# Performance work log

Hardware: AMD Instinct MI355X
Metric: run time of the kernel (lower is better)

The kernel has to match this reference:

```python
import jax, jax.numpy as jnp
import numpy as np

B, N, C = 2, 1024, 768
H = 12            # num_heads
HP = 24           # H_prime
HD = C // H       # head_dim = 64
KS = 3            # local conv kernel size
SCALE = HD ** -0.5


def setup_inputs() -> dict:
    key = jax.random.key(0)
    ks = jax.random.split(key, 9)
    s = lambda fan_in: 1.0 / np.sqrt(fan_in)
    return {
        "x": jax.random.normal(ks[0], (B, N, C), jnp.float32),
        "W_qk": jax.random.normal(ks[1], (2 * C, C), jnp.float32) * s(C),
        "W_v": jax.random.normal(ks[2], (C, C), jnp.float32) * s(C),
        "W_exp": jax.random.normal(ks[3], (HP, H), jnp.float32) * s(H),      # 1x1 conv H->HP
        "W_loc": jax.random.normal(ks[4], (HP, 1, KS, KS), jnp.float32) * s(KS * KS),  # depthwise 3x3
        "b_loc": jnp.zeros((HP,), jnp.float32),
        "W_red": jax.random.normal(ks[5], (H, HP), jnp.float32) * s(HP),    # 1x1 conv HP->H
        "W_proj": jax.random.normal(ks[6], (C, C), jnp.float32) * s(C),
        "b_proj": jnp.zeros((C,), jnp.float32),
    }


def _forward(x, W_qk, W_v, W_exp, W_loc, b_loc, W_red, W_proj, b_proj):
    b, n, c = x.shape
    # Attention: qk projection -> (2,B,H,N,HD)
    qk = (x @ W_qk.T).reshape(b, n, 2, H, HD).transpose(2, 0, 3, 1, 4)
    q, k = qk[0], qk[1]                                   # (B,H,N,HD)
    v = (x @ W_v.T).reshape(b, n, H, HD).transpose(0, 2, 1, 3)  # (B,H,N,HD)
    attn = jax.nn.softmax(jnp.einsum('bhnd,bhmd->bhnm', q, k) * SCALE, axis=-1)  # (B,H,N,N)

    # TokenSelector: conv-based reweighting of the attention map
    A_exp = jnp.einsum('oi,binm->bonm', W_exp, attn)      # 1x1 expand -> (B,HP,N,N)
    A_loc = jax.lax.conv_general_dilated(
        A_exp, W_loc, window_strides=(1, 1), padding='SAME',
        dimension_numbers=('NCHW', 'OIHW', 'NCHW'),
        feature_group_count=HP) + b_loc[None, :, None, None]
    A_loc = jax.nn.relu(A_loc)
    A_red = jnp.einsum('oi,binm->bonm', W_red, A_loc) * SCALE  # (B,H,N,N)
    attn2 = jax.nn.softmax(A_red, axis=-1)

    out = jnp.einsum('bhnm,bhmd->bhnd', attn2, v)         # (B,H,N,HD)
    out = out.transpose(0, 2, 1, 3).reshape(b, n, c)      # (B,N,C)
    out = out @ W_proj.T + b_proj
    return out, A_exp


def reference(x, W_qk, W_v, W_exp, W_loc, b_loc, W_red, W_proj, b_proj):
    return _forward(x, W_qk, W_v, W_exp, W_loc, b_loc, W_red, W_proj, b_proj)
```

## Files before the change

kernel.cpp:

```cpp
#include <hip/hip_runtime.h>
#include <math.h>

#define BB    2
#define NN    1024
#define CC    768
#define HH    12
#define HPP   24
#define HD    64
#define SCALE 0.125f

typedef float fvec4 __attribute__((ext_vector_type(4)));

#define SEG   (2*1024*768)
#define QOFF  0
#define KOFF  (SEG)
#define VOFF  (2*SEG)
#define HOFF  (3*SEG)

__global__ __launch_bounds__(256)
void qkv_gemm(const float* __restrict__ x, const float* __restrict__ Wqk,
              const float* __restrict__ Wv, float* __restrict__ ws)
{
    __shared__ float As[16][68];
    __shared__ float Bs[16][68];
    float* qtok = ws + QOFF;
    float* kt   = ws + KOFF;
    float* vws  = ws + VOFF;

    const int tid  = threadIdx.x;
    const int bn   = blockIdx.x;
    const int bm   = blockIdx.y;
    const int tx   = tid & 15, ty = tid >> 4;
    const int lrow = tid >> 2;
    const int lk   = (tid & 3) << 2;

    const int jrow = bn * 64 + lrow;
    const float* Bsrc = (jrow < 1536) ? (Wqk + (size_t)jrow * 768)
                                      : (Wv  + (size_t)(jrow - 1536) * 768);
    const float* Asrc = x + (size_t)(bm * 64 + lrow) * 768;

    float c[4][4] = {};

    for (int k0 = 0; k0 < 768; k0 += 16) {
        float4 av = *(const float4*)(Asrc + k0 + lk);
        float4 bv = *(const float4*)(Bsrc + k0 + lk);
        __syncthreads();
        As[lk+0][lrow] = av.x; As[lk+1][lrow] = av.y;
        As[lk+2][lrow] = av.z; As[lk+3][lrow] = av.w;
        Bs[lk+0][lrow] = bv.x; Bs[lk+1][lrow] = bv.y;
        Bs[lk+2][lrow] = bv.z; Bs[lk+3][lrow] = bv.w;
        __syncthreads();
#pragma unroll
        for (int kk = 0; kk < 16; ++kk) {
            float a[4], b[4];
#pragma unroll
            for (int i = 0; i < 4; ++i) a[i] = As[kk][ty*4 + i];
#pragma unroll
            for (int j = 0; j < 4; ++j) b[j] = Bs[kk][tx*4 + j];
#pragma unroll
            for (int i = 0; i < 4; ++i)
#pragma unroll
                for (int j = 0; j < 4; ++j)
                    c[i][j] = fmaf(a[i], b[j], c[i][j]);
        }
    }

#pragma unroll
    for (int i = 0; i < 4; ++i) {
        const int t = bm*64 + ty*4 + i;
        const int b = t >> 10, n = t & 1023;
#pragma unroll
        for (int j = 0; j < 4; ++j) {
            const int col = bn*64 + tx*4 + j;
            const float val = c[i][j];
            if (col < 768) {
                qtok[(size_t)t*768 + col] = val;
            } else if (col < 1536) {
                const int p = col - 768;
                kt[((size_t)(b*768 + p))*NN + n] = val;
            } else {
                const int p = col - 1536;
                vws[(((size_t)b*HH + (p >> 6))*NN + n)*HD + (p & 63)] = val;
            }
        }
    }
}

__global__ __launch_bounds__(256, 4)
void attn_expand(const float* __restrict__ qtok, const float* __restrict__ kt,
                 const float* __restrict__ Wexp, float* __restrict__ aexp)
{
    __shared__ __align__(16) float qs[2*CC];
    __shared__ float wexp_s[HPP * HH];
    __shared__ float smax[2][HH * 4];
    __shared__ float ssum[2][HH * 4];

    const int tid  = threadIdx.x;
    const int lane = tid & 63, wid = tid >> 6;
    const int x    = blockIdx.x & 7;
    const int b    = x >> 2;
    const int np   = ((x & 3) << 7) | (blockIdx.x >> 3);
    const int n0   = np << 1;
    const int m4   = tid;

    const fvec4* qsrc = (const fvec4*)(qtok + (size_t)(b*NN + n0) * CC);
    ((fvec4*)qs)[tid] = qsrc[tid];
    if (tid < 128) ((fvec4*)qs)[256 + tid] = qsrc[256 + tid];
    for (int i2 = tid; i2 < HPP*HH; i2 += 256) wexp_s[i2] = Wexp[i2];
    __syncthreads();

    fvec4 l0[HH], l1[HH];
#pragma unroll
    for (int h = 0; h < HH; ++h) {
        fvec4 a0 = {0.f,0.f,0.f,0.f}, a1 = {0.f,0.f,0.f,0.f};
        const fvec4* kr = ((const fvec4*)kt) + (size_t)(b*768 + h*64) * 256 + m4;
        const float* q0p = qs + h*64;
        const float* q1p = qs + CC + h*64;
#pragma unroll 8
        for (int d = 0; d < 64; ++d) {
            const fvec4 kv = kr[(size_t)d * 256];
            const float qa = q0p[d];
            const float qb = q1p[d];
            a0.x = fmaf(kv.x, qa, a0.x); a0.y = fmaf(kv.y, qa, a0.y);
            a0.z = fmaf(kv.z, qa, a0.z); a0.w = fmaf(kv.w, qa, a0.w);
            a1.x = fmaf(kv.x, qb, a1.x); a1.y = fmaf(kv.y, qb, a1.y);
            a1.z = fmaf(kv.z, qb, a1.z); a1.w = fmaf(kv.w, qb, a1.w);
        }
        l0[h].x = a0.x*SCALE; l0[h].y = a0.y*SCALE;
        l0[h].z = a0.z*SCALE; l0[h].w = a0.w*SCALE;
        l1[h].x = a1.x*SCALE; l1[h].y = a1.y*SCALE;
        l1[h].z = a1.z*SCALE; l1[h].w = a1.w*SCALE;
    }

#pragma unroll
    for (int h = 0; h < HH; ++h) {
        float t0 = fmaxf(fmaxf(l0[h].x, l0[h].y), fmaxf(l0[h].z, l0[h].w));
        float t1 = fmaxf(fmaxf(l1[h].x, l1[h].y), fmaxf(l1[h].z, l1[h].w));
#pragma unroll
        for (int off = 32; off > 0; off >>= 1) {
            t0 = fmaxf(t0, __shfl_xor(t0, off, 64));
            t1 = fmaxf(t1, __shfl_xor(t1, off, 64));
        }
        if (lane == 0) { smax[0][h*4 + wid] = t0; smax[1][h*4 + wid] = t1; }
    }
    __syncthreads();

#pragma unroll
    for (int h = 0; h < HH; ++h) {
        const float m0 = fmaxf(fmaxf(smax[0][h*4+0], smax[0][h*4+1]),
                               fmaxf(smax[0][h*4+2], smax[0][h*4+3]));
        const float m1 = fmaxf(fmaxf(smax[1][h*4+0], smax[1][h*4+1]),
                               fmaxf(smax[1][h*4+2], smax[1][h*4+3]));
        l0[h].x = __expf(l0[h].x - m0); l0[h].y = __expf(l0[h].y - m0);
        l0[h].z = __expf(l0[h].z - m0); l0[h].w = __expf(l0[h].w - m0);
        l1[h].x = __expf(l1[h].x - m1); l1[h].y = __expf(l1[h].y - m1);
        l1[h].z = __expf(l1[h].z - m1); l1[h].w = __expf(l1[h].w - m1);
        float s0 = (l0[h].x + l0[h].y) + (l0[h].z + l0[h].w);
        float s1 = (l1[h].x + l1[h].y) + (l1[h].z + l1[h].w);
#pragma unroll
        for (int off = 32; off > 0; off >>= 1) {
            s0 += __shfl_xor(s0, off, 64);
            s1 += __shfl_xor(s1, off, 64);
        }
        if (lane == 0) { ssum[0][h*4 + wid] = s0; ssum[1][h*4 + wid] = s1; }
    }
    __syncthreads();

#pragma unroll
    for (int h = 0; h < HH; ++h) {
        const float i0 = 1.f / (ssum[0][h*4+0] + ssum[0][h*4+1] +
                                ssum[0][h*4+2] + ssum[0][h*4+3]);
        const float i1 = 1.f / (ssum[1][h*4+0] + ssum[1][h*4+1] +
                                ssum[1][h*4+2] + ssum[1][h*4+3]);
        l0[h].x *= i0; l0[h].y *= i0; l0[h].z *= i0; l0[h].w *= i0;
        l1[h].x *= i1; l1[h].y *= i1; l1[h].z *= i1; l1[h].w *= i1;
    }

    fvec4* ab = ((fvec4*)aexp) + ((size_t)b*HPP*NN + n0) * 256;
#pragma unroll 4
    for (int o = 0; o < HPP; ++o) {
        fvec4 e0 = {0.f,0.f,0.f,0.f}, e1 = {0.f,0.f,0.f,0.f};
#pragma unroll
        for (int h = 0; h < HH; ++h) {
            const float w = wexp_s[o*HH + h];
            e0.x = fmaf(w, l0[h].x, e0.x); e0.y = fmaf(w, l0[h].y, e0.y);
            e0.z = fmaf(w, l0[h].z, e0.z); e0.w = fmaf(w, l0[h].w, e0.w);
            e1.x = fmaf(w, l1[h].x, e1.x); e1.y = fmaf(w, l1[h].y, e1.y);
            e1.z = fmaf(w, l1[h].z, e1.z); e1.w = fmaf(w, l1[h].w, e1.w);
        }
        fvec4* p0 = ab + (size_t)o * NN * 256 + m4;
        __builtin_nontemporal_store(e0, p0);
        __builtin_nontemporal_store(e1, p0 + 256);
    }
}

#define ROWSTR 1040
#define BUFSTR (3*ROWSTR)

__global__ __launch_bounds__(256, 3)
void conv_red_pv(const float* __restrict__ aexp, const float* __restrict__ Wloc,
                 const float* __restrict__ bloc, const float* __restrict__ Wred,
                 const float* __restrict__ vws, float* __restrict__ hout)
{
    __shared__ float smem[HH * NN];
    __shared__ float wloc_s[HPP * 9];
    __shared__ float bloc_s[HPP];
    __shared__ float wred_s[HH * HPP];
    __shared__ float redbuf[HH * 4];

    const int tid  = threadIdx.x;
    const int lane = tid & 63, wid = tid >> 6;
    const int x    = blockIdx.x & 7;
    const int b    = x >> 2;
    const int n    = ((x & 3) << 8) | (blockIdx.x >> 3);

    for (int idx = tid; idx < HPP*9; idx += 256) wloc_s[idx] = Wloc[idx];
    if (tid < HPP) bloc_s[tid] = bloc[tid];
    for (int idx = tid; idx < HH*HPP; idx += 256) wred_s[idx] = Wred[idx] * SCALE;
    if (tid < 12) {
        const int bu = tid / 6, rr = (tid % 6) / 2, cell = tid & 1;
        smem[bu*BUFSTR + rr*ROWSTR + (cell ? 1028 : 3)] = 0.f;
    }

    const bool rv[3] = { n > 0, true, n < NN-1 };

    float4 ld[3];
#pragma unroll
    for (int r = 0; r < 3; ++r) {
        if (rv[r]) {
            const size_t row = ((size_t)(b*HPP + 0)*NN + (n-1+r));
            ld[r] = ((const float4*)aexp)[row*256 + tid];
        } else ld[r] = make_float4(0.f,0.f,0.f,0.f);
    }
#pragma unroll
    for (int r = 0; r < 3; ++r)
        *((float4*)(smem + 0*BUFSTR + r*ROWSTR + 4) + tid) = ld[r];

    float4 acc[HH];
#pragma unroll
    for (int i = 0; i < HH; ++i) acc[i] = make_float4(0.f,0.f,0.f,0.f);

    for (int o = 0; o < HPP; ++o) {
        const int buf = o & 1;
        if (o < HPP-1) {
#pragma unroll
            for (int r = 0; r < 3; ++r) {
                if (rv[r]) {
                    const size_t row = ((size_t)(b*HPP + (o+1))*NN + (n-1+r));
                    ld[r] = ((const float4*)aexp)[row*256 + tid];
                } else ld[r] = make_float4(0.f,0.f,0.f,0.f);
            }
        }
        __syncthreads();

        const float* w  = wloc_s + o*9;
        const float  bb = bloc_s[o];
        const float* r0 = smem + buf*BUFSTR + 0*ROWSTR + 3 + 4*tid;
        const float* r1 = smem + buf*BUFSTR + 1*ROWSTR + 3 + 4*tid;
        const float* r2 = smem + buf*BUFSTR + 2*ROWSTR + 3 + 4*tid;

        float val[4];
#pragma unroll
        for (int j = 0; j < 4; ++j) {
            float a = bb;
            a = fmaf(r0[j+0], w[0], a); a = fmaf(r0[j+1], w[1], a); a = fmaf(r0[j+2], w[2], a);
            a = fmaf(r1[j+0], w[3], a); a = fmaf(r1[j+1], w[4], a); a = fmaf(r1[j+2], w[5], a);
            a = fmaf(r2[j+0], w[6], a); a = fmaf(r2[j+1], w[7], a); a = fmaf(r2[j+2], w[8], a);
            val[j] = fmaxf(a, 0.f);
        }
#pragma unroll
        for (int i = 0; i < HH; ++i) {
            const float wr = wred_s[i*HPP + o];
            acc[i].x = fmaf(wr, val[0], acc[i].x);
            acc[i].y = fmaf(wr, val[1], acc[i].y);
            acc[i].z = fmaf(wr, val[2], acc[i].z);
            acc[i].w = fmaf(wr, val[3], acc[i].w);
        }
        if (o < HPP-1) {
#pragma unroll
            for (int r = 0; r < 3; ++r)
                *((float4*)(smem + (buf^1)*BUFSTR + r*ROWSTR + 4) + tid) = ld[r];
        }
    }

#pragma unroll
    for (int i = 0; i < HH; ++i) {
        float t = fmaxf(fmaxf(acc[i].x, acc[i].y), fmaxf(acc[i].z, acc[i].w));
#pragma unroll
        for (int off = 32; off > 0; off >>= 1) t = fmaxf(t, __shfl_xor(t, off, 64));
        if (lane == 0) redbuf[i*4 + wid] = t;
    }
    __syncthreads();
    float mh[HH];
#pragma unroll
    for (int i = 0; i < HH; ++i)
        mh[i] = fmaxf(fmaxf(redbuf[i*4+0], redbuf[i*4+1]),
                      fmaxf(redbuf[i*4+2], redbuf[i*4+3]));
    __syncthreads();

#pragma unroll
    for (int i = 0; i < HH; ++i) {
        acc[i].x = __expf(acc[i].x - mh[i]);
        acc[i].y = __expf(acc[i].y - mh[i]);
        acc[i].z = __expf(acc[i].z - mh[i]);
        acc[i].w = __expf(acc[i].w - mh[i]);
        float s = (acc[i].x + acc[i].y) + (acc[i].z + acc[i].w);
#pragma unroll
        for (int off = 32; off > 0; off >>= 1) s += __shfl_xor(s, off, 64);
        if (lane == 0) redbuf[i*4 + wid] = s;
    }
    __syncthreads();
#pragma unroll
    for (int i = 0; i < HH; ++i) {
        const float inv = 1.f / (redbuf[i*4+0] + redbuf[i*4+1] +
                                 redbuf[i*4+2] + redbuf[i*4+3]);
        acc[i].x *= inv; acc[i].y *= inv; acc[i].z *= inv; acc[i].w *= inv;
        ((float4*)smem)[i*256 + tid] = acc[i];
    }
    __syncthreads();

    const int mg = lane >> 4, dq = lane & 15;
    const size_t outbase = ((size_t)(b*NN + n)) * CC;
#pragma unroll
    for (int t = 0; t < 3; ++t) {
        const int i = wid*3 + t;
        const float4* vp = (const float4*)(vws + (((size_t)b*HH + i)*NN)*HD) + dq;
        const float*  pr = smem + i*NN + mg;
        float4 a4 = make_float4(0.f,0.f,0.f,0.f);
#pragma unroll 8
        for (int m0 = 0; m0 < NN; m0 += 4) {
            const float  p  = pr[m0];
            const float4 vv = vp[(size_t)(m0+mg)*16];
            a4.x = fmaf(p, vv.x, a4.x);
            a4.y = fmaf(p, vv.y, a4.y);
            a4.z = fmaf(p, vv.z, a4.z);
            a4.w = fmaf(p, vv.w, a4.w);
        }
        a4.x += __shfl_xor(a4.x, 16, 64); a4.x += __shfl_xor(a4.x, 32, 64);
        a4.y += __shfl_xor(a4.y, 16, 64); a4.y += __shfl_xor(a4.y, 32, 64);
        a4.z += __shfl_xor(a4.z, 16, 64); a4.z += __shfl_xor(a4.z, 32, 64);
        a4.w += __shfl_xor(a4.w, 16, 64); a4.w += __shfl_xor(a4.w, 32, 64);
        if (mg == 0)
            ((float4*)(hout + outbase + i*HD))[dq] = a4;
    }
}

__global__ __launch_bounds__(256)
void proj_gemm(const float* __restrict__ A, const float* __restrict__ Wp,
               const float* __restrict__ bias, float* __restrict__ out)
{
    __shared__ float As[16][68];
    __shared__ float Bs[16][68];

    const int tid  = threadIdx.x;
    const int bn   = blockIdx.x;
    const int bm   = blockIdx.y;
    const int tx   = tid & 15, ty = tid >> 4;
    const int lrow = tid >> 2;
    const int lk   = (tid & 3) << 2;

    const float* Asrc = A  + (size_t)(bm*64 + lrow) * 768;
    const float* Bsrc = Wp + (size_t)(bn*64 + lrow) * 768;

    float c[4][4] = {};

    for (int k0 = 0; k0 < 768; k0 += 16) {
        float4 av = *(const float4*)(Asrc + k0 + lk);
        float4 bv = *(const float4*)(Bsrc + k0 + lk);
        __syncthreads();
        As[lk+0][lrow] = av.x; As[lk+1][lrow] = av.y;
        As[lk+2][lrow] = av.z; As[lk+3][lrow] = av.w;
        Bs[lk+0][lrow] = bv.x; Bs[lk+1][lrow] = bv.y;
        Bs[lk+2][lrow] = bv.z; Bs[lk+3][lrow] = bv.w;
        __syncthreads();
#pragma unroll
        for (int kk = 0; kk < 16; ++kk) {
            float a[4], b[4];
#pragma unroll
            for (int i = 0; i < 4; ++i) a[i] = As[kk][ty*4 + i];
#pragma unroll
            for (int j = 0; j < 4; ++j) b[j] = Bs[kk][tx*4 + j];
#pragma unroll
            for (int i = 0; i < 4; ++i)
#pragma unroll
                for (int j = 0; j < 4; ++j)
                    c[i][j] = fmaf(a[i], b[j], c[i][j]);
        }
    }

#pragma unroll
    for (int i = 0; i < 4; ++i) {
        const int t = bm*64 + ty*4 + i;
#pragma unroll
        for (int j = 0; j < 4; ++j) {
            const int col = bn*64 + tx*4 + j;
            out[(size_t)t*768 + col] = c[i][j] + bias[col];
        }
    }
}

extern "C" void kernel_launch(void* const* d_in, const int* in_sizes, int n_in,
                              void* d_out, int out_size, void* d_ws, size_t ws_size,
                              hipStream_t stream)
{
    const float* x     = (const float*)d_in[0];
    const float* Wqk   = (const float*)d_in[1];
    const float* Wv    = (const float*)d_in[2];
    const float* Wexp  = (const float*)d_in[3];
    const float* Wloc  = (const float*)d_in[4];
    const float* bloc  = (const float*)d_in[5];
    const float* Wred  = (const float*)d_in[6];
    const float* Wproj = (const float*)d_in[7];
    const float* bproj = (const float*)d_in[8];

    float* out  = (float*)d_out;
    float* aexp = out + (size_t)SEG;
    float* ws   = (float*)d_ws;

    qkv_gemm   <<<dim3(36, 32), 256, 0, stream>>>(x, Wqk, Wv, ws);
    attn_expand<<<dim3(BB * NN / 2), 256, 0, stream>>>(ws + QOFF, ws + KOFF, Wexp, aexp);
    conv_red_pv<<<dim3(BB * NN), 256, 0, stream>>>(aexp, Wloc, bloc, Wred,
                                                   ws + VOFF, ws + HOFF);
    proj_gemm  <<<dim3(12, 32), 256, 0, stream>>>(ws + HOFF, Wproj, bproj, out);
}
```

Measured before the change: 816.3 us.

## Process two query rows per block and compute conv halo via wave shuffles

Restructures conv_red_pv so each 512-thread block handles two adjacent rows. The 3x3 depthwise conv now reads its neighbours through wave shuffles plus global halo loads instead of a double-buffered LDS staging area, which removes the per-channel barriers. The PV product reuses each loaded V vector for both rows, halving V traffic per output row. The cost is more complex halo handling, weights read directly from global memory, and a smaller LDS footprint with different occupancy.

```diff
diff --git a/kernel.cpp b/kernel.cpp
--- a/kernel.cpp
+++ b/kernel.cpp
@@ -194,108 +194,107 @@
     }
 }
 
-#define ROWSTR 1040
-#define BUFSTR (3*ROWSTR)
-
-__global__ __launch_bounds__(256, 3)
+__global__ __launch_bounds__(512, 4)
 void conv_red_pv(const float* __restrict__ aexp, const float* __restrict__ Wloc,
                  const float* __restrict__ bloc, const float* __restrict__ Wred,
                  const float* __restrict__ vws, float* __restrict__ hout)
 {
-    __shared__ float smem[HH * NN];
-    __shared__ float wloc_s[HPP * 9];
-    __shared__ float bloc_s[HPP];
-    __shared__ float wred_s[HH * HPP];
-    __shared__ float redbuf[HH * 4];
+    __shared__ __align__(16) float probs[8][NN];
+    __shared__ float redbuf[2][HH][4];
 
     const int tid  = threadIdx.x;
-    const int lane = tid & 63, wid = tid >> 6;
-    const int x    = blockIdx.x & 7;
-    const int b    = x >> 2;
-    const int n    = ((x & 3) << 8) | (blockIdx.x >> 3);
-
-    for (int idx = tid; idx < HPP*9; idx += 256) wloc_s[idx] = Wloc[idx];
-    if (tid < HPP) bloc_s[tid] = bloc[tid];
-    for (int idx = tid; idx < HH*HPP; idx += 256) wred_s[idx] = Wred[idx] * SCALE;
-    if (tid < 12) {
-        const int bu = tid / 6, rr = (tid % 6) / 2, cell = tid & 1;
-        smem[bu*BUFSTR + rr*ROWSTR + (cell ? 1028 : 3)] = 0.f;
-    }
-
-    const bool rv[3] = { n > 0, true, n < NN-1 };
-
-    float4 ld[3];
-#pragma unroll
-    for (int r = 0; r < 3; ++r) {
-        if (rv[r]) {
-            const size_t row = ((size_t)(b*HPP + 0)*NN + (n-1+r));
-            ld[r] = ((const float4*)aexp)[row*256 + tid];
-        } else ld[r] = make_float4(0.f,0.f,0.f,0.f);
-    }
-#pragma unroll
-    for (int r = 0; r < 3; ++r)
-        *((float4*)(smem + 0*BUFSTR + r*ROWSTR + 4) + tid) = ld[r];
+    const int lane = tid & 63;
+    const int w    = tid >> 6;
+    const int tk   = w >> 2;
+    const int wq   = w & 3;
+    const int t    = tid & 255;
+
+    const int x  = blockIdx.x & 7;
+    const int b  = x >> 2;
+    const int np = ((x & 3) << 7) | (blockIdx.x >> 3);
+    const int n0 = np << 1;
+    const int n  = n0 + tk;
+
+    const bool rv0 = n > 0, rv2 = n < NN - 1;
 
     float4 acc[HH];
 #pragma unroll
     for (int i = 0; i < HH; ++i) acc[i] = make_float4(0.f,0.f,0.f,0.f);
 
+    auto loadch = [&](int o, float4 ld[3], float hl[3], float hr[3]) {
+        const float* cb = aexp + ((size_t)(b*HPP + o) * NN + (size_t)(n-1)) * NN;
+#pragma unroll
+        for (int r = 0; r < 3; ++r) {
+            const bool ok = (r == 0) ? rv0 : (r == 2 ? rv2 : true);
+            const float* rp = cb + (size_t)r * NN;
+            if (ok) {
+                ld[r] = ((const float4*)rp)[t];
+                hl[r] = (lane == 0  && wq > 0) ? rp[4*t - 1] : 0.f;
+                hr[r] = (lane == 63 && wq < 3) ? rp[4*t + 4] : 0.f;
+            } else {
+                ld[r] = make_float4(0.f,0.f,0.f,0.f);
+                hl[r] = 0.f; hr[r] = 0.f;
+            }
+        }
+    };
+
+    float4 ld[3]; float hl[3], hr[3];
+    loadch(0, ld, hl, hr);
+
     for (int o = 0; o < HPP; ++o) {
-        const int buf = o & 1;
+        float4 l2[3]; float h2l[3], h2r[3];
+        if (o < HPP-1) loadch(o+1, l2, h2l, h2r);
+
+        const float* wl = Wloc + o*9;
+        const float  bb = bloc[o];
+        float v0 = bb, v1 = bb, v2 = bb, v3 = bb;
+#pragma unroll
+        for (int r = 0; r < 3; ++r) {
+            const float w0 = wl[r*3+0], w1 = wl[r*3+1], w2 = wl[r*3+2];
+            const float4 c = ld[r];
+            float lf = __shfl_up(c.w, 1, 64);
+            float rt = __shfl_down(c.x, 1, 64);
+            if (lane == 0)  lf = hl[r];
+            if (lane == 63) rt = hr[r];
+            v0 = fmaf(w0, lf,  v0); v0 = fmaf(w1, c.x, v0); v0 = fmaf(w2, c.y, v0);
+            v1 = fmaf(w0, c.x, v1); v1 = fmaf(w1, c.y, v1); v1 = fmaf(w2, c.z, v1);
+            v2 = fmaf(w0, c.y, v2); v2 = fmaf(w1, c.z, v2); v2 = fmaf(w2, c.w, v2);
+            v3 = fmaf(w0, c.z, v3); v3 = fmaf(w1, c.w, v3); v3 = fmaf(w2, rt,  v3);
+        }
+        v0 = fmaxf(v0, 0.f); v1 = fmaxf(v1, 0.f);
+        v2 = fmaxf(v2, 0.f); v3 = fmaxf(v3, 0.f);
+#pragma unroll
+        for (int i = 0; i < HH; ++i) {
+            const float wr = Wred[i*HPP + o];
+            acc[i].x = fmaf(wr, v0, acc[i].x);
+            acc[i].y = fmaf(wr, v1, acc[i].y);
+            acc[i].z = fmaf(wr, v2, acc[i].z);
+            acc[i].w = fmaf(wr, v3, acc[i].w);
+        }
         if (o < HPP-1) {
 #pragma unroll
-            for (int r = 0; r < 3; ++r) {
-                if (rv[r]) {
-                    const size_t row = ((size_t)(b*HPP + (o+1))*NN + (n-1+r));
-                    ld[r] = ((const float4*)aexp)[row*256 + tid];
-                } else ld[r] = make_float4(0.f,0.f,0.f,0.f);
-            }
-        }
-        __syncthreads();
-
-        const float* w  = wloc_s + o*9;
-        const float  bb = bloc_s[o];
-        const float* r0 = smem + buf*BUFSTR + 0*ROWSTR + 3 + 4*tid;
-        const float* r1 = smem + buf*BUFSTR + 1*ROWSTR + 3 + 4*tid;
-        const float* r2 = smem + buf*BUFSTR + 2*ROWSTR + 3 + 4*tid;
-
-        float val[4];
-#pragma unroll
-        for (int j = 0; j < 4; ++j) {
-            float a = bb;
-            a = fmaf(r0[j+0], w[0], a); a = fmaf(r0[j+1], w[1], a); a = fmaf(r0[j+2], w[2], a);
-            a = fmaf(r1[j+0], w[3], a); a = fmaf(r1[j+1], w[4], a); a = fmaf(r1[j+2], w[5], a);
-            a = fmaf(r2[j+0], w[6], a); a = fmaf(r2[j+1], w[7], a); a = fmaf(r2[j+2], w[8], a);
-            val[j] = fmaxf(a, 0.f);
-        }
-#pragma unroll
-        for (int i = 0; i < HH; ++i) {
-            const float wr = wred_s[i*HPP + o];
-            acc[i].x = fmaf(wr, val[0], acc[i].x);
-            acc[i].y = fmaf(wr, val[1], acc[i].y);
-            acc[i].z = fmaf(wr, val[2], acc[i].z);
-            acc[i].w = fmaf(wr, val[3], acc[i].w);
-        }
-        if (o < HPP-1) {
-#pragma unroll
-            for (int r = 0; r < 3; ++r)
-                *((float4*)(smem + (buf^1)*BUFSTR + r*ROWSTR + 4) + tid) = ld[r];
-        }
-    }
-
+            for (int r = 0; r < 3; ++r) { ld[r]=l2[r]; hl[r]=h2l[r]; hr[r]=h2r[r]; }
+        }
+    }
 #pragma unroll
     for (int i = 0; i < HH; ++i) {
-        float t = fmaxf(fmaxf(acc[i].x, acc[i].y), fmaxf(acc[i].z, acc[i].w));
-#pragma unroll
-        for (int off = 32; off > 0; off >>= 1) t = fmaxf(t, __shfl_xor(t, off, 64));
-        if (lane == 0) redbuf[i*4 + wid] = t;
+        acc[i].x *= SCALE; acc[i].y *= SCALE;
+        acc[i].z *= SCALE; acc[i].w *= SCALE;
+    }
+
+#pragma unroll
+    for (int i = 0; i < HH; ++i) {
+        float tm = fmaxf(fmaxf(acc[i].x, acc[i].y), fmaxf(acc[i].z, acc[i].w));
+#pragma unroll
+        for (int off = 32; off > 0; off >>= 1) tm = fmaxf(tm, __shfl_xor(tm, off, 64));
+        if (lane == 0) redbuf[tk][i][wq] = tm;
     }
     __syncthreads();
     float mh[HH];
 #pragma unroll
     for (int i = 0; i < HH; ++i)
-        mh[i] = fmaxf(fmaxf(redbuf[i*4+0], redbuf[i*4+1]),
-                      fmaxf(redbuf[i*4+2], redbuf[i*4+3]));
+        mh[i] = fmaxf(fmaxf(redbuf[tk][i][0], redbuf[tk][i][1]),
+                      fmaxf(redbuf[tk][i][2], redbuf[tk][i][3]));
     __syncthreads();
 
 #pragma unroll
@@ -307,41 +306,56 @@
         float s = (acc[i].x + acc[i].y) + (acc[i].z + acc[i].w);
 #pragma unroll
         for (int off = 32; off > 0; off >>= 1) s += __shfl_xor(s, off, 64);
-        if (lane == 0) redbuf[i*4 + wid] = s;
+        if (lane == 0) redbuf[tk][i][wq] = s;
     }
     __syncthreads();
 #pragma unroll
     for (int i = 0; i < HH; ++i) {
-        const float inv = 1.f / (redbuf[i*4+0] + redbuf[i*4+1] +
-                                 redbuf[i*4+2] + redbuf[i*4+3]);
+        const float inv = 1.f / (redbuf[tk][i][0] + redbuf[tk][i][1] +
+                                 redbuf[tk][i][2] + redbuf[tk][i][3]);
         acc[i].x *= inv; acc[i].y *= inv; acc[i].z *= inv; acc[i].w *= inv;
-        ((float4*)smem)[i*256 + tid] = acc[i];
-    }
-    __syncthreads();
-
-    const int mg = lane >> 4, dq = lane & 15;
-    const size_t outbase = ((size_t)(b*NN + n)) * CC;
-#pragma unroll
-    for (int t = 0; t < 3; ++t) {
-        const int i = wid*3 + t;
-        const float4* vp = (const float4*)(vws + (((size_t)b*HH + i)*NN)*HD) + dq;
-        const float*  pr = smem + i*NN + mg;
-        float4 a4 = make_float4(0.f,0.f,0.f,0.f);
+    }
+
+    const int hq = w >> 1;
+    const int dh = w & 1;
+    const int mg = lane >> 3;
+    const int dq = lane & 7;
+
+    for (int g = 0; g < 3; ++g) {
+        __syncthreads();
+#pragma unroll
+        for (int q2 = 0; q2 < 4; ++q2)
+            ((float4*)&probs[q2*2 + tk][0])[t] = acc[4*g + q2];
+        __syncthreads();
+
+        const int h = 4*g + hq;
+        const float4* vp = ((const float4*)vws)
+                         + ((size_t)(b*HH + h) * NN) * 16 + dh*8 + dq;
+        const float* p0 = &probs[hq*2 + 0][0] + mg;
+        const float* p1 = &probs[hq*2 + 1][0] + mg;
+        float4 a0 = make_float4(0.f,0.f,0.f,0.f);
+        float4 a1 = make_float4(0.f,0.f,0.f,0.f);
 #pragma unroll 8
-        for (int m0 = 0; m0 < NN; m0 += 4) {
-            const float  p  = pr[m0];
-            const float4 vv = vp[(size_t)(m0+mg)*16];
-            a4.x = fmaf(p, vv.x, a4.x);
-            a4.y = fmaf(p, vv.y, a4.y);
-            a4.z = fmaf(p, vv.z, a4.z);
-            a4.w = fmaf(p, vv.w, a4.w);
-        }
-        a4.x += __shfl_xor(a4.x, 16, 64); a4.x += __shfl_xor(a4.x, 32, 64);
-        a4.y += __shfl_xor(a4.y, 16, 64); a4.y += __shfl_xor(a4.y, 32, 64);
-        a4.z += __shfl_xor(a4.z, 16, 64); a4.z += __shfl_xor(a4.z, 32, 64);
-        a4.w += __shfl_xor(a4.w, 16, 64); a4.w += __shfl_xor(a4.w, 32, 64);
-        if (mg == 0)
-            ((float4*)(hout + outbase + i*HD))[dq] = a4;
+        for (int m0 = 0; m0 < NN; m0 += 8) {
+            const float  pa = p0[m0];
+            const float  pb = p1[m0];
+            const float4 vv = vp[(size_t)(m0 + mg) * 16];
+            a0.x = fmaf(pa, vv.x, a0.x); a0.y = fmaf(pa, vv.y, a0.y);
+            a0.z = fmaf(pa, vv.z, a0.z); a0.w = fmaf(pa, vv.w, a0.w);
+            a1.x = fmaf(pb, vv.x, a1.x); a1.y = fmaf(pb, vv.y, a1.y);
+            a1.z = fmaf(pb, vv.z, a1.z); a1.w = fmaf(pb, vv.w, a1.w);
+        }
+#pragma unroll
+        for (int off = 8; off < 64; off <<= 1) {
+            a0.x += __shfl_xor(a0.x, off, 64); a0.y += __shfl_xor(a0.y, off, 64);
+            a0.z += __shfl_xor(a0.z, off, 64); a0.w += __shfl_xor(a0.w, off, 64);
+            a1.x += __shfl_xor(a1.x, off, 64); a1.y += __shfl_xor(a1.y, off, 64);
+            a1.z += __shfl_xor(a1.z, off, 64); a1.w += __shfl_xor(a1.w, off, 64);
+        }
+        if (mg == 0) {
+            ((float4*)(hout + ((size_t)(b*NN + n0    ) * CC) + h*HD))[dh*8 + dq] = a0;
+            ((float4*)(hout + ((size_t)(b*NN + n0 + 1) * CC) + h*HD))[dh*8 + dq] = a1;
+        }
     }
 }
 
@@ -419,7 +433,7 @@
 
     qkv_gemm   <<<dim3(36, 32), 256, 0, stream>>>(x, Wqk, Wv, ws);
     attn_expand<<<dim3(BB * NN / 2), 256, 0, stream>>>(ws + QOFF, ws + KOFF, Wexp, aexp);
-    conv_red_pv<<<dim3(BB * NN), 256, 0, stream>>>(aexp, Wloc, bloc, Wred,
-                                                   ws + VOFF, ws + HOFF);
+    conv_red_pv<<<dim3(BB * NN / 2), 512, 0, stream>>>(aexp, Wloc, bloc, Wred,
+                                                       ws + VOFF, ws + HOFF);
     proj_gemm  <<<dim3(12, 32), 256, 0, stream>>>(ws + HOFF, Wproj, bproj, out);
 }
```

After: 768.9 us. 5.8% less time.
